# Performance work log

Hardware: AMD Instinct MI355X
Metric: run time of the kernel (lower is better)

## Reference

```python
import jax, jax.numpy as jnp
import numpy as np

N = 100_000   # nodes
E = 3_200_000 # edges (avg degree 32)

def _glorot(k, shape):
    fan_in, fan_out = shape
    lim = float(np.sqrt(6.0 / (fan_in + fan_out)))
    return jax.random.uniform(k, shape, jnp.float32, -lim, lim)

def setup_inputs() -> dict:
    key = jax.random.key(0)
    ks = jax.random.split(key, 8)
    x = jax.random.normal(ks[0], (N, 3), dtype=jnp.float32)
    edge_index = jax.random.randint(ks[1], (2, E), 0, N, dtype=jnp.int32)
    choices = jax.random.bernoulli(ks[2], 0.5, (N,))
    W1 = _glorot(ks[3], (3, 16));  b1 = jnp.zeros((16,), jnp.float32)
    W2 = _glorot(ks[4], (16, 16)); b2 = jnp.zeros((16,), jnp.float32)
    W3 = _glorot(ks[5], (16, 1));  b3 = jnp.zeros((1,), jnp.float32)
    fc_w = _glorot(ks[6], (16, 1)); fc_b = jnp.zeros((1,), jnp.float32)
    return dict(x=x, edge_index=edge_index, choices=choices,
                W1=W1, b1=b1, W2=W2, b2=b2, W3=W3, b3=b3,
                fc_w=fc_w, fc_b=fc_b)

def reference(x, edge_index, choices, W1, b1, W2, b2, W3, b3, fc_w, fc_b):
    row, col = edge_index[0], edge_index[1]  # source -> target
    # improved=True GCN norm: self-loop weight 2, deg = in_degree + 2
    deg = jax.ops.segment_sum(jnp.ones((E,), x.dtype), col, num_segments=N) + 2.0
    dinv = jax.lax.rsqrt(deg)                    # [N]
    enorm = dinv[row] * dinv[col]                # [E] edge normalization
    self_norm = 2.0 * dinv * dinv                # [N] self-loop term

    def gcn(h, W, b):
        h = h @ W                                # [N, F_out]
        agg = jax.ops.segment_sum(h[row] * enorm[:, None], col, num_segments=N)
        return agg + self_norm[:, None] * h + b

    h = jax.nn.relu(gcn(x, W1, b1))
    h = jax.nn.relu(gcn(h, W2, b2))
    c = gcn(h, W3, b3)[:, 0]                     # [N] per-node logit
    # masked softmax over chosen nodes (torch masked_select + softmax,
    # expressed with static shape: non-chosen entries get probability 0)
    logits = jnp.where(choices, c, -jnp.inf)
    choice = jax.nn.softmax(logits, axis=0)      # [N]
    # global_mean_pool with a single graph = mean over all nodes
    v = jnp.mean(h, axis=0, keepdims=True)       # [1, 16]
    value = v @ fc_w + fc_b                      # [1, 1]
    return choice, value
```

## Files before the change

### kernel.cpp

```cpp
#include <hip/hip_runtime.h>
#include <hip/hip_fp16.h>
#include <math.h>

#define BLK 256


#define BSH 8
#define NB 512
#define EB 8192
#define BINTH 512

__device__ inline float4 load_h4(const __half* base, int node, int sub) {
    const uint2* p = reinterpret_cast<const uint2*>(base + ((size_t)node << 4)) + sub;
    uint2 u = *p;
    union { unsigned u; __half2 h; } a, b;
    a.u = u.x; b.u = u.y;
    float2 fa = __half22float2(a.h), fb = __half22float2(b.h);
    return make_float4(fa.x, fa.y, fb.x, fb.y);
}

__device__ inline void store_h4(__half* base, int node, int sub, float4 v) {
    union { unsigned u; __half2 h; } a, b;
    a.h = __floats2half2_rn(v.x, v.y);
    b.h = __floats2half2_rn(v.z, v.w);
    uint2 u; u.x = a.u; u.y = b.u;
    *(reinterpret_cast<uint2*>(base + ((size_t)node << 4)) + sub) = u;
}

__device__ inline float3 load_xs(const __half* xs, int node) {
    uint2 u = *reinterpret_cast<const uint2*>(xs + ((size_t)node << 2));
    union { unsigned u; __half2 h; } a, b;
    a.u = u.x; b.u = u.y;
    float2 fa = __half22float2(a.h), fb = __half22float2(b.h);
    return make_float3(fa.x, fa.y, fb.x);
}

__global__ void __launch_bounds__(BLK) k_bcount(const int* __restrict__ col,
                                                int* __restrict__ bcnt, int E) {
    __shared__ int hist[NB];
    int tid = threadIdx.x;
    int base = blockIdx.x * EB;
    int cnt = min(EB, E - base);
    hist[tid] = 0; hist[tid + 256] = 0;
    __syncthreads();
    for (int j = tid; j < cnt; j += BLK)
        atomicAdd(&hist[col[base + j] >> BSH], 1);
    __syncthreads();
    if (hist[tid] > 0) atomicAdd(&bcnt[tid], hist[tid]);
    if (hist[tid + 256] > 0) atomicAdd(&bcnt[tid + 256], hist[tid + 256]);
}

__global__ void __launch_bounds__(NB) k_bscan(const int* __restrict__ bcnt,
                                              int* __restrict__ gcur,
                                              int* __restrict__ bbase, int nbuck) {
    __shared__ int s[NB];
    int tid = threadIdx.x;
    int v = (tid < nbuck) ? bcnt[tid] : 0;
    s[tid] = v;
    __syncthreads();
    for (int d = 1; d < NB; d <<= 1) {
        int t = (tid >= d) ? s[tid - d] : 0;
        __syncthreads();
        if (tid >= d) s[tid] += t;
        __syncthreads();
    }
    int ex = s[tid] - v;
    gcur[tid] = ex;
    bbase[tid] = ex;
}

__global__ void __launch_bounds__(BINTH) k_bin(const int* __restrict__ row,
                                               const int* __restrict__ col,
                                               int* __restrict__ gcur,
                                               int* __restrict__ packed, int E) {
    __shared__ int stage[EB];
    __shared__ unsigned short sbuk[EB];
    __shared__ int hist[NB];
    __shared__ int lscan[NB];
    __shared__ int cur[NB];
    __shared__ int gbase[NB];
    int tid = threadIdx.x;
    int base = blockIdx.x * EB;
    int cnt = min(EB, E - base);

    hist[tid] = 0;
    __syncthreads();
    for (int j = tid; j < cnt; j += BINTH) {
        int c = __builtin_nontemporal_load(col + base + j);
        atomicAdd(&hist[c >> BSH], 1);
    }
    __syncthreads();
    lscan[tid] = hist[tid];
    __syncthreads();
    for (int d = 1; d < NB; d <<= 1) {
        int t = (tid >= d) ? lscan[tid - d] : 0;
        __syncthreads();
        if (tid >= d) lscan[tid] += t;
        __syncthreads();
    }
    {
        int ex = lscan[tid] - hist[tid];
        lscan[tid] = ex;
        cur[tid] = ex;
    }
    __syncthreads();
    for (int j = tid; j < cnt; j += BINTH) {
        int c = __builtin_nontemporal_load(col + base + j);
        int r = __builtin_nontemporal_load(row + base + j);
        int b = c >> BSH;
        int p = atomicAdd(&cur[b], 1);
        stage[p] = (r << BSH) | (c & ((1 << BSH) - 1));
        sbuk[p] = (unsigned short)b;
    }
    __syncthreads();
    if (hist[tid] > 0) gbase[tid] = atomicAdd(&gcur[tid], hist[tid]);
    __syncthreads();
    for (int j = tid; j < cnt; j += BINTH) {
        int b = sbuk[j];
        int pos = gbase[b] + (j - lscan[b]);
        packed[pos] = stage[j];
    }
}

__global__ void __launch_bounds__(BLK) k_place(const int* __restrict__ packed,
                                               const int* __restrict__ bbase,
                                               const int* __restrict__ bcnt,
                                               const float* __restrict__ x,
                                               int* __restrict__ degi,
                                               int* __restrict__ offs,
                                               float* __restrict__ dinv,
                                               __half* __restrict__ xs,
                                               int* __restrict__ srcs, int n) {
    __shared__ int cnt[256];
    __shared__ int lcur[256];
    __shared__ int ssum[256];
    int tid = threadIdx.x;
    int b = blockIdx.x;
    int nb0 = b << BSH;
    cnt[tid] = 0;
    __syncthreads();
    int pbeg = bbase[b];
    int ecnt = bcnt[b];
    for (int j = tid; j < ecnt; j += BLK)
        atomicAdd(&cnt[packed[pbeg + j] & 255], 1);
    __syncthreads();
    int c = cnt[tid];
    ssum[tid] = c;
    __syncthreads();
    for (int d = 1; d < 256; d <<= 1) {
        int t = (tid >= d) ? ssum[tid - d] : 0;
        __syncthreads();
        if (tid >= d) ssum[tid] += t;
        __syncthreads();
    }
    int ex = ssum[tid] - c;
    lcur[tid] = ex;
    int i = nb0 + tid;
    if (i < n) {
        degi[i] = c;
        offs[i] = pbeg + ex;
        float di = rsqrtf((float)c + 2.0f);
        dinv[i] = di;
        float x0 = x[i * 3 + 0], x1 = x[i * 3 + 1], x2 = x[i * 3 + 2];
        union { unsigned u; __half2 h; } a2, b2;
        a2.h = __floats2half2_rn(di * x0, di * x1);
        b2.h = __floats2half2_rn(di * x2, 0.f);
        uint2 u; u.x = a2.u; u.y = b2.u;
        *reinterpret_cast<uint2*>(xs + ((size_t)i << 2)) = u;
    }
    __syncthreads();
    for (int j = tid; j < ecnt; j += BLK) {
        int v = packed[pbeg + j];
        int li = v & 255;
        int r = v >> BSH;
        int slot = atomicAdd(&lcur[li], 1);
        srcs[pbeg + slot] = r;
    }
}

__global__ void __launch_bounds__(BLK) k_agg1(const __half* __restrict__ xs,
                                              const int* __restrict__ offs,
                                              const int* __restrict__ degi,
                                              const int* __restrict__ srcs,
                                              const float* __restrict__ dinv,
                                              const float* __restrict__ b1,
                                              const float* __restrict__ W1,
                                              const float* __restrict__ W2,
                                              __half* __restrict__ hwsB, int n) {
    __shared__ float w1[48];
    __shared__ float w2[256];
    __shared__ float bb[16];
    __shared__ float hbuf[64][17];
    int tid = threadIdx.x;
    w2[tid] = W2[tid];
    if (tid < 48) w1[tid] = W1[tid];
    if (tid < 16) bb[tid] = b1[tid];
    __syncthreads();
    int nl = tid >> 2, sub = tid & 3;
    int i = blockIdx.x * 64 + nl;
    bool act = (i < n);
    float di = 0.f;
    if (act) {
        di = dinv[i];
        float ax = 0.f, ay = 0.f, az = 0.f;
        float bx = 0.f, by = 0.f, bz = 0.f;
        int beg = offs[i], end = beg + degi[i];
        int j = beg + sub;
        for (; j + 12 < end; j += 16) {
            int r0 = srcs[j], r1 = srcs[j + 4], r2 = srcs[j + 8], r3 = srcs[j + 12];
            float3 q0 = load_xs(xs, r0);
            float3 q1 = load_xs(xs, r1);
            float3 q2 = load_xs(xs, r2);
            float3 q3 = load_xs(xs, r3);
            ax += q0.x; ay += q0.y; az += q0.z;
            bx += q1.x; by += q1.y; bz += q1.z;
            ax += q2.x; ay += q2.y; az += q2.z;
            bx += q3.x; by += q3.y; bz += q3.z;
        }
        for (; j < end; j += 4) {
            float3 q0 = load_xs(xs, srcs[j]);
            ax += q0.x; ay += q0.y; az += q0.z;
        }
        ax += bx; ay += by; az += bz;
        ax += __shfl_xor(ax, 1); ay += __shfl_xor(ay, 1); az += __shfl_xor(az, 1);
        ax += __shfl_xor(ax, 2); ay += __shfl_xor(ay, 2); az += __shfl_xor(az, 2);
        float3 s = load_xs(xs, i);
        ax += 2.f * s.x; ay += 2.f * s.y; az += 2.f * s.z;
#pragma unroll
        for (int k = 0; k < 4; k++) {
            int f = sub * 4 + k;
            float hv = di * (ax * w1[f] + ay * w1[16 + f] + az * w1[32 + f]) + bb[f];
            hbuf[nl][f] = fmaxf(hv, 0.f);
        }
    }
    __syncthreads();
    if (act) {
        const float* hn = hbuf[nl];
        float s0 = 0.f, s1 = 0.f, s2 = 0.f, s3 = 0.f;
#pragma unroll
        for (int f = 0; f < 16; f++) {
            float hv = hn[f];
            const float4 wq = *(const float4*)&w2[f * 16 + sub * 4];
            s0 += hv * wq.x; s1 += hv * wq.y; s2 += hv * wq.z; s3 += hv * wq.w;
        }
        store_h4(hwsB, i, sub, make_float4(di * s0, di * s1, di * s2, di * s3));
    }
}

#define GATHER4H(HWS)                                                           \
    float4 acc;                                                                 \
    {                                                                           \
        float4 s0 = load_h4(HWS, i, sub);                                       \
        acc = make_float4(2.f * s0.x, 2.f * s0.y, 2.f * s0.z, 2.f * s0.w);      \
        float4 a1 = make_float4(0.f, 0.f, 0.f, 0.f);                            \
        float4 a2 = a1, a3 = a1;                                                \
        int beg = offs[i], end = beg + degi[i];                                 \
        int j = beg;                                                            \
        for (; j + 3 < end; j += 4) {                                           \
            int r0 = srcs[j], r1 = srcs[j + 1], r2 = srcs[j + 2], r3 = srcs[j + 3]; \
            float4 q0 = load_h4(HWS, r0, sub);                                  \
            float4 q1 = load_h4(HWS, r1, sub);                                  \
            float4 q2 = load_h4(HWS, r2, sub);                                  \
            float4 q3 = load_h4(HWS, r3, sub);                                  \
            acc.x += q0.x; acc.y += q0.y; acc.z += q0.z; acc.w += q0.w;         \
            a1.x += q1.x; a1.y += q1.y; a1.z += q1.z; a1.w += q1.w;             \
            a2.x += q2.x; a2.y += q2.y; a2.z += q2.z; a2.w += q2.w;             \
            a3.x += q3.x; a3.y += q3.y; a3.z += q3.z; a3.w += q3.w;             \
        }                                                                       \
        for (; j < end; j++) {                                                  \
            float4 q0 = load_h4(HWS, srcs[j], sub);                             \
            acc.x += q0.x; acc.y += q0.y; acc.z += q0.z; acc.w += q0.w;         \
        }                                                                       \
        acc.x += a1.x + a2.x + a3.x;                                            \
        acc.y += a1.y + a2.y + a3.y;                                            \
        acc.z += a1.z + a2.z + a3.z;                                            \
        acc.w += a1.w + a2.w + a3.w;                                            \
    }

__global__ void __launch_bounds__(BLK) k_agg2(const __half* __restrict__ hwsB,
                                              const int* __restrict__ offs,
                                              const int* __restrict__ degi,
                                              const int* __restrict__ srcs,
                                              const float* __restrict__ dinv,
                                              const float* __restrict__ b2,
                                              const float* __restrict__ W3,
                                              float* __restrict__ hws3,
                                              float* __restrict__ pool, int n) {
    __shared__ float w3[16];
    __shared__ float bb[16];
    __shared__ float lp[16];
    int tid = threadIdx.x;
    if (tid < 16) { w3[tid] = W3[tid]; bb[tid] = b2[tid]; lp[tid] = 0.f; }
    __syncthreads();
    int nl = tid >> 2, sub = tid & 3;
    int i = blockIdx.x * 64 + nl;
    bool act = (i < n);
    float4 h = make_float4(0.f, 0.f, 0.f, 0.f);
    if (act) {
        float di = dinv[i];
        GATHER4H(hwsB);
        h.x = fmaxf(di * acc.x + bb[sub * 4 + 0], 0.f);
        h.y = fmaxf(di * acc.y + bb[sub * 4 + 1], 0.f);
        h.z = fmaxf(di * acc.z + bb[sub * 4 + 2], 0.f);
        h.w = fmaxf(di * acc.w + bb[sub * 4 + 3], 0.f);
        float p = h.x * w3[sub * 4 + 0] + h.y * w3[sub * 4 + 1]
                + h.z * w3[sub * 4 + 2] + h.w * w3[sub * 4 + 3];
        p += __shfl_xor(p, 1);
        p += __shfl_xor(p, 2);
        if (sub == 0) hws3[i] = di * p;
    }
    float4 hp = h;
#pragma unroll
    for (int m = 4; m < 64; m <<= 1) {
        hp.x += __shfl_xor(hp.x, m);
        hp.y += __shfl_xor(hp.y, m);
        hp.z += __shfl_xor(hp.z, m);
        hp.w += __shfl_xor(hp.w, m);
    }
    if ((tid & 63) < 4) {
        atomicAdd(&lp[sub * 4 + 0], hp.x);
        atomicAdd(&lp[sub * 4 + 1], hp.y);
        atomicAdd(&lp[sub * 4 + 2], hp.z);
        atomicAdd(&lp[sub * 4 + 3], hp.w);
    }
    __syncthreads();
    if (tid < 16) atomicAdd(&pool[tid], lp[tid]);
}

__global__ void __launch_bounds__(BLK) k_agg3(const float* __restrict__ hws3,
                                              const int* __restrict__ offs,
                                              const int* __restrict__ degi,
                                              const int* __restrict__ srcs,
                                              const float* __restrict__ dinv,
                                              const float* __restrict__ b3,
                                              const int* __restrict__ choices,
                                              float* __restrict__ cbuf,
                                              float* __restrict__ pmax, int n) {
    __shared__ float red[BLK];
    int tid = threadIdx.x;
    int nl = tid >> 2, sub = tid & 3;
    int i = blockIdx.x * 64 + nl;
    bool act = (i < n);
    float s = 0.f;
    if (act) {
        int beg = offs[i], end = beg + degi[i];
        for (int j = beg + sub; j < end; j += 4) s += hws3[srcs[j]];
    }
    s += __shfl_xor(s, 1);
    s += __shfl_xor(s, 2);
    float logit = -INFINITY;
    if (act && sub == 0) {
        float c = dinv[i] * (s + 2.f * hws3[i]) + b3[0];
        cbuf[i] = c;
        if (choices[i] != 0) logit = c;
    }
    red[tid] = logit;
    __syncthreads();
    for (int d = BLK / 2; d > 0; d >>= 1) {
        if (tid < d) red[tid] = fmaxf(red[tid], red[tid + d]);
        __syncthreads();
    }
    if (tid == 0) pmax[blockIdx.x] = red[0];
}

__global__ void k_redmax(const float* __restrict__ pmax, float* __restrict__ scal_m, int nblk) {
    __shared__ float red[BLK];
    float m = -INFINITY;
    for (int i = threadIdx.x; i < nblk; i += BLK) m = fmaxf(m, pmax[i]);
    red[threadIdx.x] = m;
    __syncthreads();
    for (int d = BLK / 2; d > 0; d >>= 1) {
        if (threadIdx.x < d) red[threadIdx.x] = fmaxf(red[threadIdx.x], red[threadIdx.x + d]);
        __syncthreads();
    }
    if (threadIdx.x == 0) scal_m[0] = red[0];
}

__global__ void __launch_bounds__(BLK) k_sumexp(const float* __restrict__ cbuf,
                                                const int* __restrict__ choices,
                                                const float* __restrict__ scal_m,
                                                float* __restrict__ Ssum, int n) {
    __shared__ float red[BLK];
    int i = blockIdx.x * BLK + threadIdx.x;
    float m = scal_m[0];
    float v = 0.0f;
    if (i < n && choices[i] != 0) v = expf(cbuf[i] - m);
    red[threadIdx.x] = v;
    __syncthreads();
    for (int d = BLK / 2; d > 0; d >>= 1) {
        if (threadIdx.x < d) red[threadIdx.x] += red[threadIdx.x + d];
        __syncthreads();
    }
    if (threadIdx.x == 0) atomicAdd(Ssum, red[0]);
}

__global__ void __launch_bounds__(BLK) k_final(const float* __restrict__ cbuf,
                                               const int* __restrict__ choices,
                                               const float* __restrict__ scal_m,
                                               const float* __restrict__ Ssum,
                                               const float* __restrict__ pool,
                                               const float* __restrict__ fcw,
                                               const float* __restrict__ fcb,
                                               float* __restrict__ out, int n) {
    int i = blockIdx.x * BLK + threadIdx.x;
    if (i < n) {
        float p = 0.0f;
        if (choices[i] != 0) {
            float m = scal_m[0], S = Ssum[0];
            p = expf(cbuf[i] - m) / S;
        }
        out[i] = p;
    }
    if (blockIdx.x == 0 && threadIdx.x == 0) {
        float invn = 1.0f / (float)n;
        float v = 0.0f;
#pragma unroll
        for (int f = 0; f < 16; f++) v += (pool[f] * invn) * fcw[f];
        out[n] = v + fcb[0];
    }
}

extern "C" void kernel_launch(void* const* d_in, const int* in_sizes, int n_in,
                              void* d_out, int out_size, void* d_ws, size_t ws_size,
                              hipStream_t stream) {
    const float* x       = (const float*)d_in[0];
    const int*   ei      = (const int*)d_in[1];
    const int*   choices = (const int*)d_in[2];
    const float* W1 = (const float*)d_in[3];
    const float* b1 = (const float*)d_in[4];
    const float* W2 = (const float*)d_in[5];
    const float* b2 = (const float*)d_in[6];
    const float* W3 = (const float*)d_in[7];
    const float* b3 = (const float*)d_in[8];
    const float* fcw = (const float*)d_in[9];
    const float* fcb = (const float*)d_in[10];
    float* out = (float*)d_out;

    int n = in_sizes[0] / 3;
    int E = in_sizes[1] / 2;
    const int* row = ei;
    const int* col = ei + E;

    int nblkN = (n + BLK - 1) / BLK;
    int nblk64 = (n + 63) / 64;
    int nbuck = (n + (1 << BSH) - 1) >> BSH;
    int nblkBin = (E + EB - 1) / EB;

    char* ws = (char*)d_ws;
    size_t o = 0;
    auto alloc = [&](size_t bytes) { char* p = ws + o; o += (bytes + 15) & ~(size_t)15; return p; };
    int*   degi   = (int*)  alloc((size_t)n * 4);
    int*   offs   = (int*)  alloc((size_t)n * 4);
    float* dinv   = (float*)alloc((size_t)n * 4);
    float* hws3   = (float*)alloc((size_t)n * 4);
    float* cbuf   = (float*)alloc((size_t)n * 4);
    float* pmax   = (float*)alloc(16384);
    int*   bcnt   = (int*)  alloc(NB * 4);
    int*   gcur   = (int*)  alloc(NB * 4);
    int*   bbase  = (int*)  alloc(NB * 4);
    float* scal   = (float*)alloc(256);
    float* Ssum   = scal + 0;
    float* pool   = scal + 1;
    float* scal_m = scal + 17;
    __half* xs    = (__half*)alloc((size_t)n * 4 * 2);
    size_t hw_bytes = (size_t)n * 16 * 2;
    size_t pk_bytes = (size_t)E * 4;
    char*  blob   = alloc(hw_bytes > pk_bytes ? hw_bytes : pk_bytes);
    int*    packed = (int*)blob;
    __half* hwsB   = (__half*)blob;
    int*   srcs   = (int*)  alloc((size_t)E * 4);
    (void)ws_size;

    hipMemsetAsync(bcnt, 0, NB * 4, stream);
    hipMemsetAsync(scal, 0, 68, stream);

    k_bcount<<<nblkBin, BLK, 0, stream>>>(col, bcnt, E);
    k_bscan<<<1, NB, 0, stream>>>(bcnt, gcur, bbase, nbuck);
    k_bin<<<nblkBin, BINTH, 0, stream>>>(row, col, gcur, packed, E);
    k_place<<<nbuck, BLK, 0, stream>>>(packed, bbase, bcnt, x, degi, offs, dinv, xs, srcs, n);

    k_agg1<<<nblk64, BLK, 0, stream>>>(xs, offs, degi, srcs, dinv, b1, W1, W2, hwsB, n);
    k_agg2<<<nblk64, BLK, 0, stream>>>(hwsB, offs, degi, srcs, dinv, b2, W3, hws3, pool, n);
    k_agg3<<<nblk64, BLK, 0, stream>>>(hws3, offs, degi, srcs, dinv, b3, choices, cbuf, pmax, n);

    k_redmax<<<1, BLK, 0, stream>>>(pmax, scal_m, nblk64);
    k_sumexp<<<nblkN, BLK, 0, stream>>>(cbuf, choices, scal_m, Ssum, n);
    k_final<<<nblkN, BLK, 0, stream>>>(cbuf, choices, scal_m, Ssum, pool, fcw, fcb, out, n);
}
```

Baseline: 261.0 us.

## Drop bucket count pass with fixed-capacity buckets and fuse max reduction via atomicMax

Binning now writes edges into fixed-capacity per-bucket slots (CAP 10240 per 256-node bucket). This removes the separate edge-counting and scan kernels and their read of the column indices. k_place now computes each bucket's global offset by summing the preceding bucket counts itself. The softmax max is reduced with an order-preserving encoded atomicMax, which removes the k_redmax launch. The gather loops are unrolled further (8-wide for 16-feature layers, 2-wide for the scalar layer) to keep more loads in flight. The capacity assumption fails silently if any 256-node bucket receives more than 10240 incoming edges.

```diff
diff --git a/kernel.cpp b/kernel.cpp
--- a/kernel.cpp
+++ b/kernel.cpp
@@ -7,6 +7,7 @@
 
 #define BSH 8
 #define NB 512
+#define CAP 10240
 #define EB 8192
 #define BINTH 512
 
@@ -35,38 +36,19 @@
     return make_float3(fa.x, fa.y, fb.x);
 }
 
-__global__ void __launch_bounds__(BLK) k_bcount(const int* __restrict__ col,
-                                                int* __restrict__ bcnt, int E) {
-    __shared__ int hist[NB];
-    int tid = threadIdx.x;
-    int base = blockIdx.x * EB;
-    int cnt = min(EB, E - base);
-    hist[tid] = 0; hist[tid + 256] = 0;
-    __syncthreads();
-    for (int j = tid; j < cnt; j += BLK)
-        atomicAdd(&hist[col[base + j] >> BSH], 1);
-    __syncthreads();
-    if (hist[tid] > 0) atomicAdd(&bcnt[tid], hist[tid]);
-    if (hist[tid + 256] > 0) atomicAdd(&bcnt[tid + 256], hist[tid + 256]);
-}
-
-__global__ void __launch_bounds__(NB) k_bscan(const int* __restrict__ bcnt,
-                                              int* __restrict__ gcur,
-                                              int* __restrict__ bbase, int nbuck) {
-    __shared__ int s[NB];
-    int tid = threadIdx.x;
-    int v = (tid < nbuck) ? bcnt[tid] : 0;
-    s[tid] = v;
-    __syncthreads();
-    for (int d = 1; d < NB; d <<= 1) {
-        int t = (tid >= d) ? s[tid - d] : 0;
-        __syncthreads();
-        if (tid >= d) s[tid] += t;
-        __syncthreads();
-    }
-    int ex = s[tid] - v;
-    gcur[tid] = ex;
-    bbase[tid] = ex;
+__device__ inline unsigned encf(float f) {
+    unsigned u = __float_as_uint(f);
+    return (u & 0x80000000u) ? ~u : (u | 0x80000000u);
+}
+__device__ inline float decf(unsigned e) {
+    return (e & 0x80000000u) ? __uint_as_float(e ^ 0x80000000u)
+                             : __uint_as_float(~e);
+}
+
+__global__ void k_init(int* __restrict__ gcur, float* __restrict__ scal) {
+    int t = threadIdx.x;
+    gcur[t] = 0;
+    if (t < 18) scal[t] = 0.f;
 }
 
 __global__ void __launch_bounds__(BINTH) k_bin(const int* __restrict__ row,
@@ -113,7 +95,7 @@
         sbuk[p] = (unsigned short)b;
     }
     __syncthreads();
-    if (hist[tid] > 0) gbase[tid] = atomicAdd(&gcur[tid], hist[tid]);
+    if (hist[tid] > 0) gbase[tid] = tid * CAP + atomicAdd(&gcur[tid], hist[tid]);
     __syncthreads();
     for (int j = tid; j < cnt; j += BINTH) {
         int b = sbuk[j];
@@ -123,7 +105,6 @@
 }
 
 __global__ void __launch_bounds__(BLK) k_place(const int* __restrict__ packed,
-                                               const int* __restrict__ bbase,
                                                const int* __restrict__ bcnt,
                                                const float* __restrict__ x,
                                                int* __restrict__ degi,
@@ -134,15 +115,23 @@
     __shared__ int cnt[256];
     __shared__ int lcur[256];
     __shared__ int ssum[256];
+    __shared__ int psum[256];
     int tid = threadIdx.x;
     int b = blockIdx.x;
-    int nb0 = b << BSH;
+    int pv = 0;
+    for (int t = tid; t < b; t += BLK) pv += bcnt[t];
+    psum[tid] = pv;
     cnt[tid] = 0;
     __syncthreads();
-    int pbeg = bbase[b];
+    for (int d = BLK / 2; d > 0; d >>= 1) {
+        if (tid < d) psum[tid] += psum[tid + d];
+        __syncthreads();
+    }
+    int pbeg = psum[0];
     int ecnt = bcnt[b];
+    const int* pk = packed + (size_t)b * CAP;
     for (int j = tid; j < ecnt; j += BLK)
-        atomicAdd(&cnt[packed[pbeg + j] & 255], 1);
+        atomicAdd(&cnt[pk[j] & 255], 1);
     __syncthreads();
     int c = cnt[tid];
     ssum[tid] = c;
@@ -155,7 +144,7 @@
     }
     int ex = ssum[tid] - c;
     lcur[tid] = ex;
-    int i = nb0 + tid;
+    int i = (b << BSH) + tid;
     if (i < n) {
         degi[i] = c;
         offs[i] = pbeg + ex;
@@ -170,11 +159,10 @@
     }
     __syncthreads();
     for (int j = tid; j < ecnt; j += BLK) {
-        int v = packed[pbeg + j];
+        int v = pk[j];
         int li = v & 255;
-        int r = v >> BSH;
         int slot = atomicAdd(&lcur[li], 1);
-        srcs[pbeg + slot] = r;
+        srcs[pbeg + slot] = v >> BSH;
     }
 }
 
@@ -247,7 +235,7 @@
     }
 }
 
-#define GATHER4H(HWS)                                                           \
+#define GATHER8H(HWS)                                                           \
     float4 acc;                                                                 \
     {                                                                           \
         float4 s0 = load_h4(HWS, i, sub);                                       \
@@ -256,16 +244,25 @@
         float4 a2 = a1, a3 = a1;                                                \
         int beg = offs[i], end = beg + degi[i];                                 \
         int j = beg;                                                            \
-        for (; j + 3 < end; j += 4) {                                           \
-            int r0 = srcs[j], r1 = srcs[j + 1], r2 = srcs[j + 2], r3 = srcs[j + 3]; \
+        for (; j + 7 < end; j += 8) {                                           \
+            int r0 = srcs[j],     r1 = srcs[j + 1], r2 = srcs[j + 2], r3 = srcs[j + 3]; \
+            int r4 = srcs[j + 4], r5 = srcs[j + 5], r6 = srcs[j + 6], r7 = srcs[j + 7]; \
             float4 q0 = load_h4(HWS, r0, sub);                                  \
             float4 q1 = load_h4(HWS, r1, sub);                                  \
             float4 q2 = load_h4(HWS, r2, sub);                                  \
             float4 q3 = load_h4(HWS, r3, sub);                                  \
-            acc.x += q0.x; acc.y += q0.y; acc.z += q0.z; acc.w += q0.w;         \
-            a1.x += q1.x; a1.y += q1.y; a1.z += q1.z; a1.w += q1.w;             \
-            a2.x += q2.x; a2.y += q2.y; a2.z += q2.z; a2.w += q2.w;             \
-            a3.x += q3.x; a3.y += q3.y; a3.z += q3.z; a3.w += q3.w;             \
+            float4 q4 = load_h4(HWS, r4, sub);                                  \
+            float4 q5 = load_h4(HWS, r5, sub);                                  \
+            float4 q6 = load_h4(HWS, r6, sub);                                  \
+            float4 q7 = load_h4(HWS, r7, sub);                                  \
+            acc.x += q0.x + q4.x; acc.y += q0.y + q4.y;                         \
+            acc.z += q0.z + q4.z; acc.w += q0.w + q4.w;                         \
+            a1.x += q1.x + q5.x; a1.y += q1.y + q5.y;                           \
+            a1.z += q1.z + q5.z; a1.w += q1.w + q5.w;                           \
+            a2.x += q2.x + q6.x; a2.y += q2.y + q6.y;                           \
+            a2.z += q2.z + q6.z; a2.w += q2.w + q6.w;                           \
+            a3.x += q3.x + q7.x; a3.y += q3.y + q7.y;                           \
+            a3.z += q3.z + q7.z; a3.w += q3.w + q7.w;                           \
         }                                                                       \
         for (; j < end; j++) {                                                  \
             float4 q0 = load_h4(HWS, srcs[j], sub);                             \
@@ -298,7 +295,7 @@
     float4 h = make_float4(0.f, 0.f, 0.f, 0.f);
     if (act) {
         float di = dinv[i];
-        GATHER4H(hwsB);
+        GATHER8H(hwsB);
         h.x = fmaxf(di * acc.x + bb[sub * 4 + 0], 0.f);
         h.y = fmaxf(di * acc.y + bb[sub * 4 + 1], 0.f);
         h.z = fmaxf(di * acc.z + bb[sub * 4 + 2], 0.f);
@@ -335,7 +332,7 @@
                                               const float* __restrict__ b3,
                                               const int* __restrict__ choices,
                                               float* __restrict__ cbuf,
-                                              float* __restrict__ pmax, int n) {
+                                              unsigned* __restrict__ menc, int n) {
     __shared__ float red[BLK];
     int tid = threadIdx.x;
     int nl = tid >> 2, sub = tid & 3;
@@ -344,7 +341,15 @@
     float s = 0.f;
     if (act) {
         int beg = offs[i], end = beg + degi[i];
-        for (int j = beg + sub; j < end; j += 4) s += hws3[srcs[j]];
+        int j = beg + sub;
+        float s1 = 0.f;
+        for (; j + 4 < end; j += 8) {
+            float q0 = hws3[srcs[j]];
+            float q1 = hws3[srcs[j + 4]];
+            s += q0; s1 += q1;
+        }
+        if (j < end) s += hws3[srcs[j]];
+        s += s1;
     }
     s += __shfl_xor(s, 1);
     s += __shfl_xor(s, 2);
@@ -360,29 +365,16 @@
         if (tid < d) red[tid] = fmaxf(red[tid], red[tid + d]);
         __syncthreads();
     }
-    if (tid == 0) pmax[blockIdx.x] = red[0];
-}
-
-__global__ void k_redmax(const float* __restrict__ pmax, float* __restrict__ scal_m, int nblk) {
-    __shared__ float red[BLK];
-    float m = -INFINITY;
-    for (int i = threadIdx.x; i < nblk; i += BLK) m = fmaxf(m, pmax[i]);
-    red[threadIdx.x] = m;
-    __syncthreads();
-    for (int d = BLK / 2; d > 0; d >>= 1) {
-        if (threadIdx.x < d) red[threadIdx.x] = fmaxf(red[threadIdx.x], red[threadIdx.x + d]);
-        __syncthreads();
-    }
-    if (threadIdx.x == 0) scal_m[0] = red[0];
+    if (tid == 0) atomicMax(menc, encf(red[0]));
 }
 
 __global__ void __launch_bounds__(BLK) k_sumexp(const float* __restrict__ cbuf,
                                                 const int* __restrict__ choices,
-                                                const float* __restrict__ scal_m,
+                                                const unsigned* __restrict__ menc,
                                                 float* __restrict__ Ssum, int n) {
     __shared__ float red[BLK];
     int i = blockIdx.x * BLK + threadIdx.x;
-    float m = scal_m[0];
+    float m = decf(*menc);
     float v = 0.0f;
     if (i < n && choices[i] != 0) v = expf(cbuf[i] - m);
     red[threadIdx.x] = v;
@@ -396,7 +388,7 @@
 
 __global__ void __launch_bounds__(BLK) k_final(const float* __restrict__ cbuf,
                                                const int* __restrict__ choices,
-                                               const float* __restrict__ scal_m,
+                                               const unsigned* __restrict__ menc,
                                                const float* __restrict__ Ssum,
                                                const float* __restrict__ pool,
                                                const float* __restrict__ fcw,
@@ -406,7 +398,7 @@
     if (i < n) {
         float p = 0.0f;
         if (choices[i] != 0) {
-            float m = scal_m[0], S = Ssum[0];
+            float m = decf(*menc), S = Ssum[0];
             p = expf(cbuf[i] - m) / S;
         }
         out[i] = p;
@@ -454,36 +446,28 @@
     float* dinv   = (float*)alloc((size_t)n * 4);
     float* hws3   = (float*)alloc((size_t)n * 4);
     float* cbuf   = (float*)alloc((size_t)n * 4);
-    float* pmax   = (float*)alloc(16384);
-    int*   bcnt   = (int*)  alloc(NB * 4);
     int*   gcur   = (int*)  alloc(NB * 4);
-    int*   bbase  = (int*)  alloc(NB * 4);
     float* scal   = (float*)alloc(256);
     float* Ssum   = scal + 0;
     float* pool   = scal + 1;
-    float* scal_m = scal + 17;
+    unsigned* menc = (unsigned*)(scal + 17);
     __half* xs    = (__half*)alloc((size_t)n * 4 * 2);
     size_t hw_bytes = (size_t)n * 16 * 2;
-    size_t pk_bytes = (size_t)E * 4;
+    size_t pk_bytes = (size_t)NB * CAP * 4;
     char*  blob   = alloc(hw_bytes > pk_bytes ? hw_bytes : pk_bytes);
     int*    packed = (int*)blob;
     __half* hwsB   = (__half*)blob;
     int*   srcs   = (int*)  alloc((size_t)E * 4);
     (void)ws_size;
 
-    hipMemsetAsync(bcnt, 0, NB * 4, stream);
-    hipMemsetAsync(scal, 0, 68, stream);
-
-    k_bcount<<<nblkBin, BLK, 0, stream>>>(col, bcnt, E);
-    k_bscan<<<1, NB, 0, stream>>>(bcnt, gcur, bbase, nbuck);
+    k_init<<<1, NB, 0, stream>>>(gcur, scal);
     k_bin<<<nblkBin, BINTH, 0, stream>>>(row, col, gcur, packed, E);
-    k_place<<<nbuck, BLK, 0, stream>>>(packed, bbase, bcnt, x, degi, offs, dinv, xs, srcs, n);
+    k_place<<<nbuck, BLK, 0, stream>>>(packed, gcur, x, degi, offs, dinv, xs, srcs, n);
 
     k_agg1<<<nblk64, BLK, 0, stream>>>(xs, offs, degi, srcs, dinv, b1, W1, W2, hwsB, n);
     k_agg2<<<nblk64, BLK, 0, stream>>>(hwsB, offs, degi, srcs, dinv, b2, W3, hws3, pool, n);
-    k_agg3<<<nblk64, BLK, 0, stream>>>(hws3, offs, degi, srcs, dinv, b3, choices, cbuf, pmax, n);
-
-    k_redmax<<<1, BLK, 0, stream>>>(pmax, scal_m, nblk64);
-    k_sumexp<<<nblkN, BLK, 0, stream>>>(cbuf, choices, scal_m, Ssum, n);
-    k_final<<<nblkN, BLK, 0, stream>>>(cbuf, choices, scal_m, Ssum, pool, fcw, fcb, out, n);
-}
+    k_agg3<<<nblk64, BLK, 0, stream>>>(hws3, offs, degi, srcs, dinv, b3, choices, cbuf, menc, n);
+
+    k_sumexp<<<nblkN, BLK, 0, stream>>>(cbuf, choices, menc, Ssum, n);
+    k_final<<<nblkN, BLK, 0, stream>>>(cbuf, choices, menc, Ssum, pool, fcw, fcb, out, n);
+}
```

Result: faster. 249.2 us (-4.5%).
